# Kernel optimization log

Measured on AMD Instinct MI355X. Metric: run time of the kernel, lower is better.

The kernel has to match this reference:

```python
import jax, jax.numpy as jnp
import numpy as np

N_QUBITS = 12
DEPTH = 3


def _apply_1q(state, U, wire, n):
    # state: [B, 2^n] complex; U: [2,2] (shared) or [B,2,2] (per-sample)
    B = state.shape[0]
    a = 2 ** wire
    c = 2 ** (n - wire - 1)
    psi = state.reshape(B, a, 2, c)
    if U.ndim == 2:
        psi = jnp.einsum('ij,bajc->baic', U, psi)
    else:
        psi = jnp.einsum('bij,bajc->baic', U, psi)
    return psi.reshape(B, -1)


def _apply_cnot(state, ctrl, tgt, n):
    B = state.shape[0]
    psi = state.reshape((B,) + (2,) * n)
    psi = jnp.moveaxis(psi, (1 + ctrl, 1 + tgt), (1, 2))
    # flip target bit on the control=1 branch
    psi = jnp.concatenate([psi[:, :1], jnp.flip(psi[:, 1:], axis=2)], axis=1)
    psi = jnp.moveaxis(psi, (1, 2), (1 + ctrl, 1 + tgt))
    return psi.reshape(B, -1)


def _ry(theta):
    # theta: [B] -> [B,2,2]
    c = jnp.cos(theta / 2)
    s = jnp.sin(theta / 2)
    return jnp.stack([jnp.stack([c, -s], -1), jnp.stack([s, c], -1)], -2).astype(jnp.complex64)


def _rot(phi, theta, omega):
    # PennyLane Rot(phi, theta, omega) = RZ(omega) @ RY(theta) @ RZ(phi)
    c = jnp.cos(theta / 2).astype(jnp.complex64)
    s = jnp.sin(theta / 2).astype(jnp.complex64)
    e = lambda a: jnp.exp(1j * a.astype(jnp.complex64))
    m00 = e(-(phi + omega) / 2) * c
    m01 = -e((phi - omega) / 2) * s
    m10 = e(-(phi - omega) / 2) * s
    m11 = e((phi + omega) / 2) * c
    return jnp.stack([jnp.stack([m00, m01]), jnp.stack([m10, m11])])


def _circuit(angles, weights, n, depth):
    # angles: [B, n] real; weights: [depth, n, 3]
    B = angles.shape[0]
    state = jnp.zeros((B, 2 ** n), jnp.complex64).at[:, 0].set(1.0)
    # RY angle encoding
    for q in range(n):
        state = _apply_1q(state, _ry(angles[:, q]), q, n)
    # StronglyEntanglingLayers: Rot on each wire, then ring CNOTs with range r
    for l in range(depth):
        for q in range(n):
            U = _rot(weights[l, q, 0], weights[l, q, 1], weights[l, q, 2])
            state = _apply_1q(state, U, q, n)
        r = l % (n - 1) + 1  # PennyLane default ranges
        for q in range(n):
            state = _apply_cnot(state, q, (q + r) % n, n)
    # PauliZ expectation on each wire
    probs = state.real ** 2 + state.imag ** 2  # [B, 2^n]
    idx = jnp.arange(2 ** n)
    bits = (idx[None, :] >> (n - 1 - jnp.arange(n)[:, None])) & 1  # wire 0 = MSB
    signs = (1.0 - 2.0 * bits).astype(probs.dtype)  # [n, 2^n]
    return probs @ signs.T  # [B, n]


def setup_inputs() -> dict:
    key = jax.random.key(0)
    ks = jax.random.split(key, 5)
    B, F, n, C = 4096, 768, N_QUBITS, 10
    x = jax.random.normal(ks[0], (B, F), jnp.float32)
    Wp = jax.random.normal(ks[1], (n, F), jnp.float32) / np.sqrt(F)
    weights = 0.01 * jax.random.normal(ks[2], (DEPTH, n, 3), jnp.float32)
    Wo = jax.random.normal(ks[3], (C, n), jnp.float32) / np.sqrt(n)
    bo = jax.random.normal(ks[4], (C,), jnp.float32) * 0.01
    return {'x': x, 'Wp': Wp, 'weights': weights, 'Wo': Wo, 'bo': bo}


def reference(x, Wp, weights, Wo, bo):
    angles = jnp.tanh(x @ Wp.T) * (np.pi / 2)  # [B, n_qubits]
    z = _circuit(angles, weights, N_QUBITS, DEPTH)  # [B, n_qubits]
    return z @ Wo.T + bo  # [B, num_classes]
```

## Files before the change

### kernel.cpp

```cpp
#include <hip/hip_runtime.h>
#include <math.h>

#define NQ 12
#define DEPTH 3
#define FEAT 768
#define NCLS 10
#define NW 8
#define AMPS 8
#define PI_HALF 1.57079632679489662f

typedef float v2f __attribute__((ext_vector_type(2)));

__device__ __forceinline__ v2f pk_mul_bl(v2f A, v2f z) {
    v2f d;
    asm("v_pk_mul_f32 %0, %1, %2 op_sel:[0,0] op_sel_hi:[1,0]"
        : "=v"(d) : "v"(A), "v"(z));
    return d;
}
__device__ __forceinline__ void pk_fma_bl(v2f& d, v2f A, v2f z) {
    asm("v_pk_fma_f32 %0, %1, %2, %0 op_sel:[0,0,0] op_sel_hi:[1,0,1]"
        : "+v"(d) : "v"(A), "v"(z));
}
__device__ __forceinline__ void pk_fma_bh(v2f& d, v2f B, v2f z) {
    asm("v_pk_fma_f32 %0, %1, %2, %0 op_sel:[0,1,0] op_sel_hi:[1,1,1]"
        : "+v"(d) : "v"(B), "v"(z));
}
__device__ __forceinline__ v2f cgate(v2f As, v2f Bs, v2f Ap, v2f Bp, v2f z, v2f p) {
    v2f d = pk_mul_bl(As, z);
    pk_fma_bh(d, Bs, z);
    pk_fma_bl(d, Ap, p);
    pk_fma_bh(d, Bp, p);
    return d;
}

#define DPPF(v, ctrl) __int_as_float(__builtin_amdgcn_update_dpp(0, __float_as_int(v), (ctrl), 0xF, 0xF, true))

template<int M>
__device__ __forceinline__ float swx(float v) {
    if constexpr (M == 1) {
        return DPPF(v, 0xB1);
    } else if constexpr (M == 2) {
        return DPPF(v, 0x4E);
    } else if constexpr (M == 4) {
        float t = DPPF(v, 0x141);
        return DPPF(t, 0x1B);
    } else if constexpr (M == 8) {
        return DPPF(v, 0x128);
    } else if constexpr (M == 16) {
        return __int_as_float(__builtin_amdgcn_ds_swizzle(__float_as_int(v), 0x401F));
    } else {
        return __shfl_xor(v, 32, 64);
    }
}

template<int M>
__device__ __forceinline__ v2f swx2(v2f z) {
    v2f p;
    p.x = swx<M>(z.x);
    p.y = swx<M>(z.y);
    return p;
}

__device__ __forceinline__ float allred(float v) {
    v += swx<1>(v); v += swx<2>(v); v += swx<4>(v);
    v += swx<8>(v); v += swx<16>(v); v += swx<32>(v);
    return v;
}


template<int JM>
__device__ __forceinline__ void rot_reg(v2f (&z)[AMPS], const v2f* m) {
    const v2f A0 = m[0], B0 = m[1], P0 = m[2], Q0 = m[3];
    const v2f A1 = m[4], B1 = m[5], P1 = m[6], Q1 = m[7];
    #pragma unroll
    for (int j = 0; j < AMPS; ++j) if (!(j & JM)) {
        const int j1 = j | JM;
        v2f z0 = z[j], z1 = z[j1];
        z[j]  = cgate(A0, B0, P0, Q0, z0, z1);
        z[j1] = cgate(A1, B1, P1, Q1, z1, z0);
    }
}

template<int LM>
__device__ __forceinline__ void rot_lane(v2f (&z)[AMPS], const v2f* m, int lane) {
    const bool b = (lane & LM) != 0;
    const v2f As = b ? m[4] : m[0], Bs = b ? m[5] : m[1];
    const v2f Ap = b ? m[6] : m[2], Bp = b ? m[7] : m[3];
    #pragma unroll
    for (int j = 0; j < AMPS; ++j) {
        v2f p = swx2<LM>(z[j]);
        z[j] = cgate(As, Bs, Ap, Bp, z[j], p);
    }
}

__device__ __forceinline__ void relayout(v2f (&z)[AMPS], v2f (*ex)[AMPS][64], int lw, int lane) {
    #pragma unroll
    for (int k = 0; k < AMPS; ++k) ex[lw][k][lane] = z[k];
    __syncthreads();
    #pragma unroll
    for (int k = 0; k < AMPS; ++k) z[k] = ex[k][lw][lane];
    __syncthreads();
}

template<int JC, int JT>
__device__ __forceinline__ void cnot_rr(v2f (&z)[AMPS]) {
    #pragma unroll
    for (int j = 0; j < AMPS; ++j) if ((j & JC) && !(j & JT)) {
        const int j1 = j | JT;
        v2f t = z[j]; z[j] = z[j1]; z[j1] = t;
    }
}

__global__ __launch_bounds__(512) void qcircuit_fz(
    const float* __restrict__ x,
    const float* __restrict__ Wp,
    const float* __restrict__ w,
    const float* __restrict__ Wo,
    const float* __restrict__ bo,
    float* __restrict__ out)
{
    const int t = threadIdx.x;
    const int wave = t >> 6;
    const int lane = t & 63;
    const int b = blockIdx.x;

    __shared__ v2f mcoef[DEPTH * NQ][8];
    __shared__ v2f ex[NW][AMPS][64];
    __shared__ float red[NW][NQ];
    __shared__ float sh_dot[NQ];
    __shared__ float sh_ac[NQ], sh_as[NQ], zsh[NQ];

    if (t < DEPTH * NQ) {
        float phi = w[t * 3 + 0], th = w[t * 3 + 1], om = w[t * 3 + 2];
        float ct = cosf(0.5f * th), sn = sinf(0.5f * th);
        float a0 = -0.5f * (phi + om);
        float a1 = 0.5f * (phi - om);
        float c0 = cosf(a0), s0 = sinf(a0);
        float c1 = cosf(a1), s1 = sinf(a1);
        float m00r = c0 * ct,  m00i = s0 * ct;
        float m01r = -c1 * sn, m01i = -s1 * sn;
        float m10r = c1 * sn,  m10i = -s1 * sn;
        float m11r = c0 * ct,  m11i = -s0 * ct;
        mcoef[t][0] = v2f{m00r, m00i};  mcoef[t][1] = v2f{-m00i, m00r};
        mcoef[t][2] = v2f{m01r, m01i};  mcoef[t][3] = v2f{-m01i, m01r};
        mcoef[t][4] = v2f{m11r, m11i};  mcoef[t][5] = v2f{-m11i, m11r};
        mcoef[t][6] = v2f{m10r, m10i};  mcoef[t][7] = v2f{-m10i, m10r};
    }

    {
        const float2* x2  = reinterpret_cast<const float2*>(x + (size_t)b * FEAT);
        const float2* Wp2 = reinterpret_cast<const float2*>(Wp);
        float2 xv[6];
        #pragma unroll
        for (int c = 0; c < 6; ++c) xv[c] = x2[lane + 64 * c];
        float accA = 0.f;
        #pragma unroll
        for (int c = 0; c < 6; ++c) {
            float2 wv = Wp2[wave * 384 + lane + 64 * c];
            accA += xv[c].x * wv.x + xv[c].y * wv.y;
        }
        accA = allred(accA);
        float accB = 0.f;
        if (wave < 4) {
            #pragma unroll
            for (int c = 0; c < 6; ++c) {
                float2 wv = Wp2[(wave + 8) * 384 + lane + 64 * c];
                accB += xv[c].x * wv.x + xv[c].y * wv.y;
            }
            accB = allred(accB);
        }
        if (lane == 0) {
            sh_dot[wave] = accA;
            if (wave < 4) sh_dot[wave + 8] = accB;
        }
    }
    __syncthreads();
    if (t < NQ) {
        float h = 0.5f * (tanhf(sh_dot[t]) * PI_HALF);
        sh_ac[t] = cosf(h);
        sh_as[t] = sinf(h);
    }
    __syncthreads();

    int lw = wave;
    float pr[AMPS];
    float L0 = ((wave & 4) ? sh_as[0] : sh_ac[0]);
    L0 *= (wave & 2) ? sh_as[1] : sh_ac[1];
    L0 *= (wave & 1) ? sh_as[2] : sh_ac[2];
    L0 *= (lane & 32) ? sh_as[3] : sh_ac[3];
    L0 *= (lane & 16) ? sh_as[4] : sh_ac[4];
    L0 *= (lane &  8) ? sh_as[5] : sh_ac[5];
    L0 *= (lane &  4) ? sh_as[6] : sh_ac[6];
    L0 *= (lane &  2) ? sh_as[7] : sh_ac[7];
    L0 *= (lane &  1) ? sh_as[8] : sh_ac[8];
    pr[0] = L0;
    #pragma unroll
    for (int wbit = 0; wbit < 3; ++wbit) {
        const int bmask = 1 << wbit;
        const float cw = sh_ac[11 - wbit], sw = sh_as[11 - wbit];
        #pragma unroll
        for (int j = 0; j < AMPS; ++j) {
            if (j < bmask) {
                pr[j | bmask] = pr[j] * sw;
                pr[j] = pr[j] * cw;
            }
        }
    }
    v2f z[AMPS];
    #pragma unroll
    for (int j = 0; j < AMPS; ++j) z[j] = v2f{pr[j], 0.f};

    {
        const v2f* mb = &mcoef[0 * NQ][0];
        rot_reg < 4>(z, mb + 9 * 8);
        rot_reg < 2>(z, mb + 10 * 8);
        rot_reg < 1>(z, mb + 11 * 8);
        rot_lane<32>(z, mb + 3 * 8, lane);
        rot_lane<16>(z, mb + 4 * 8, lane);
        rot_lane< 8>(z, mb + 5 * 8, lane);
        rot_lane< 4>(z, mb + 6 * 8, lane);
        rot_lane< 2>(z, mb + 7 * 8, lane);
        rot_lane< 1>(z, mb + 8 * 8, lane);
        relayout(z, ex, lw, lane);
        rot_reg < 4>(z, mb + 0 * 8);
        rot_reg < 2>(z, mb + 1 * 8);
        rot_reg < 1>(z, mb + 2 * 8);
        cnot_rr< 4,  2>(z);
        cnot_rr< 2,  1>(z);
        {
            const int woff = (lane & 1) << 2;
            int Ls = lane;
            Ls ^= (Ls & 2) >> 1;
            Ls ^= (Ls & 4) >> 1;
            Ls ^= (Ls & 8) >> 1;
            Ls ^= (Ls & 16) >> 1;
            Ls ^= (Ls & 32) >> 1;
            int lw2 = lw ^ ((lw & 4) ? 2 : 0);
            lw2 ^= (lw2 & 2) ? 1 : 0;
            const int wlc = (lw2 & 1) << 2;
            #pragma unroll
            for (int k = 0; k < AMPS; ++k) ex[lw][k][lane] = z[k];
            __syncthreads();
            #pragma unroll
            for (int k = 0; k < AMPS; ++k)
                z[k] = ex[lw ^ woff][k ^ wlc][Ls ^ ((k & 1) << 5)];
            __syncthreads();
            lw = lw2;
        }
    }
    {
        const v2f* mb = &mcoef[1 * NQ][0];
        rot_reg < 4>(z, mb + 0 * 8);
        rot_reg < 2>(z, mb + 1 * 8);
        rot_reg < 1>(z, mb + 2 * 8);
        rot_lane<32>(z, mb + 3 * 8, lane);
        rot_lane<16>(z, mb + 4 * 8, lane);
        rot_lane< 8>(z, mb + 5 * 8, lane);
        rot_lane< 4>(z, mb + 6 * 8, lane);
        rot_lane< 2>(z, mb + 7 * 8, lane);
        rot_lane< 1>(z, mb + 8 * 8, lane);
        relayout(z, ex, lw, lane);
        rot_reg < 4>(z, mb + 9 * 8);
        rot_reg < 2>(z, mb + 10 * 8);
        rot_reg < 1>(z, mb + 11 * 8);
        {
            lw ^= (lw & 4) >> 2;
            int Ls = lane;
            Ls ^= (Ls & 4) >> 2;
            Ls ^= (Ls & 8) >> 2;
            Ls ^= (Ls & 16) >> 2;
            Ls ^= (Ls & 32) >> 2;
            const int klx = ((lane & 2) << 1) ^ ((lane & 1) << 1);
            #pragma unroll
            for (int k = 0; k < AMPS; ++k) ex[lw][k][lane] = z[k];
            __syncthreads();
            #pragma unroll
            for (int k = 0; k < AMPS; ++k) {
                const int LW = lw ^ ((k & 1) << 1) ^ ((k & 2) << 1);
                const int K  = k ^ ((k & 4) >> 2) ^ klx;
                const int Lr = Ls ^ ((LW & 1) << 4) ^ ((LW & 2) << 4);
                z[k] = ex[LW][K][Lr];
            }
            __syncthreads();
        }
    }
    {
        const v2f* mb = &mcoef[2 * NQ][0];
        rot_reg < 4>(z, mb + 9 * 8);
        rot_reg < 2>(z, mb + 10 * 8);
        rot_reg < 1>(z, mb + 11 * 8);
        rot_lane<32>(z, mb + 3 * 8, lane);
        rot_lane<16>(z, mb + 4 * 8, lane);
        rot_lane< 8>(z, mb + 5 * 8, lane);
        rot_lane< 4>(z, mb + 6 * 8, lane);
        rot_lane< 2>(z, mb + 7 * 8, lane);
        rot_lane< 1>(z, mb + 8 * 8, lane);
        relayout(z, ex, lw, lane);
        rot_reg < 4>(z, mb + 0 * 8);
        rot_reg < 2>(z, mb + 1 * 8);
        rot_reg < 1>(z, mb + 2 * 8);
    }

    float ptot = 0.f, zn4 = 0.f, zn2 = 0.f, zn1 = 0.f;
    #pragma unroll
    for (int j = 0; j < AMPS; ++j) {
        float p = z[j].x * z[j].x + z[j].y * z[j].y;
        ptot += p;
        if (j & 4) zn4 += p;
        if (j & 2) zn2 += p;
        if (j & 1) zn1 += p;
    }
    const float S4 = ptot - 2.f * zn4;
    const float S2 = ptot - 2.f * zn2;
    const float S1 = ptot - 2.f * zn1;
    const bool p36 = ((lane >> 5) ^ (lane >> 2)) & 1;
    const bool p18 = ((lane >> 4) ^ (lane >> 1)) & 1;
    const bool p9  = ((lane >> 3) ^ lane) & 1;

    const float a0 = allred(p36 ? -ptot : ptot);
    const float a1 = allred(p18 ? -ptot : ptot);
    const float a2 = allred(p9  ? -ptot : ptot);
    const float a3 = allred((lane & 32) ? -S4 : S4);
    const float a4 = allred((lane & 16) ? -S2 : S2);
    const float a5 = allred((lane &  8) ? -S1 : S1);
    const float a6 = allred(p36 ? -S4 : S4);
    const float a7 = allred(p18 ? -S2 : S2);
    const float a8 = allred(p9  ? -S1 : S1);

    const float W9  = (lw & 4) ? -1.f : 1.f;
    const float W10 = (lw & 2) ? -1.f : 1.f;
    const float W11 = (lw & 1) ? -1.f : 1.f;
    float zp[NQ];
    zp[0]  = W9 * a0;   zp[1]  = W10 * a1;  zp[2]  = W11 * a2;
    zp[3]  = a3;        zp[4]  = a4;        zp[5]  = a5;
    zp[6]  = a6;        zp[7]  = a7;        zp[8]  = a8;
    zp[9]  = W9 * a6;   zp[10] = W10 * a7;  zp[11] = W11 * a8;

    if (lane == 0) {
        #pragma unroll
        for (int q = 0; q < NQ; ++q) red[wave][q] = zp[q];
    }
    __syncthreads();
    if (t < NQ) {
        float s = 0.f;
        #pragma unroll
        for (int v = 0; v < NW; ++v) s += red[v][t];
        zsh[t] = s;
    }
    __syncthreads();

    if (t < NCLS) {
        float o = bo[t];
        #pragma unroll
        for (int q = 0; q < NQ; ++q) o = fmaf(zsh[q], Wo[t * NQ + q], o);
        out[(size_t)b * NCLS + t] = o;
    }
}

extern "C" void kernel_launch(void* const* d_in, const int* in_sizes, int n_in,
                              void* d_out, int out_size, void* d_ws, size_t ws_size,
                              hipStream_t stream) {
    const float* x  = (const float*)d_in[0];
    const float* Wp = (const float*)d_in[1];
    const float* w  = (const float*)d_in[2];
    const float* Wo = (const float*)d_in[3];
    const float* bo = (const float*)d_in[4];
    float* out = (float*)d_out;

    const int B = in_sizes[0] / FEAT;
    qcircuit_fz<<<B, 512, 0, stream>>>(x, Wp, w, Wo, bo, out);
}
```

Before: 128.9 us.

## Use ds_swizzle lane exchange, pointer-select gate coefs, and float4 projection loads

Lane-exchange butterflies in the rotation gates now use ds_swizzle (or shfl for the 32-lane stride) for every stride, replacing the DPP variants used for strides below 16. Per-lane gate coefficients are chosen by offsetting a pointer instead of selecting each value. The input projection loads x and Wp as float4 rather than float2, halving the number of load instructions. ds_swizzle goes through the LDS crossbar, so it may add latency compared with DPP, while the wider loads reduce load instruction count.

```diff
diff --git a/kernel.cpp b/kernel.cpp
--- a/kernel.cpp
+++ b/kernel.cpp
@@ -54,11 +54,19 @@
 }
 
 template<int M>
-__device__ __forceinline__ v2f swx2(v2f z) {
-    v2f p;
-    p.x = swx<M>(z.x);
-    p.y = swx<M>(z.y);
-    return p;
+__device__ __forceinline__ v2f swxd2(v2f z) {
+    if constexpr (M == 32) {
+        v2f p;
+        p.x = __shfl_xor(z.x, 32, 64);
+        p.y = __shfl_xor(z.y, 32, 64);
+        return p;
+    } else {
+        const int off = (M << 10) | 0x1F;
+        v2f p;
+        p.x = __int_as_float(__builtin_amdgcn_ds_swizzle(__float_as_int(z.x), off));
+        p.y = __int_as_float(__builtin_amdgcn_ds_swizzle(__float_as_int(z.y), off));
+        return p;
+    }
 }
 
 __device__ __forceinline__ float allred(float v) {
@@ -83,12 +91,11 @@
 
 template<int LM>
 __device__ __forceinline__ void rot_lane(v2f (&z)[AMPS], const v2f* m, int lane) {
-    const bool b = (lane & LM) != 0;
-    const v2f As = b ? m[4] : m[0], Bs = b ? m[5] : m[1];
-    const v2f Ap = b ? m[6] : m[2], Bp = b ? m[7] : m[3];
+    const v2f* mm = m + (((lane & LM) != 0) ? 4 : 0);
+    const v2f As = mm[0], Bs = mm[1], Ap = mm[2], Bp = mm[3];
     #pragma unroll
     for (int j = 0; j < AMPS; ++j) {
-        v2f p = swx2<LM>(z[j]);
+        v2f p = swxd2<LM>(z[j]);
         z[j] = cgate(As, Bs, Ap, Bp, z[j], p);
     }
 }
@@ -111,7 +118,7 @@
     }
 }
 
-__global__ __launch_bounds__(512) void qcircuit_fz(
+__global__ __launch_bounds__(512) void qcircuit_fz2(
     const float* __restrict__ x,
     const float* __restrict__ Wp,
     const float* __restrict__ w,
@@ -148,24 +155,24 @@
     }
 
     {
-        const float2* x2  = reinterpret_cast<const float2*>(x + (size_t)b * FEAT);
-        const float2* Wp2 = reinterpret_cast<const float2*>(Wp);
-        float2 xv[6];
-        #pragma unroll
-        for (int c = 0; c < 6; ++c) xv[c] = x2[lane + 64 * c];
+        const float4* x4  = reinterpret_cast<const float4*>(x + (size_t)b * FEAT);
+        const float4* Wp4 = reinterpret_cast<const float4*>(Wp);
+        float4 xv[3];
+        #pragma unroll
+        for (int c = 0; c < 3; ++c) xv[c] = x4[lane + 64 * c];
         float accA = 0.f;
         #pragma unroll
-        for (int c = 0; c < 6; ++c) {
-            float2 wv = Wp2[wave * 384 + lane + 64 * c];
-            accA += xv[c].x * wv.x + xv[c].y * wv.y;
+        for (int c = 0; c < 3; ++c) {
+            float4 wv = Wp4[wave * 192 + lane + 64 * c];
+            accA += xv[c].x * wv.x + xv[c].y * wv.y + xv[c].z * wv.z + xv[c].w * wv.w;
         }
         accA = allred(accA);
         float accB = 0.f;
         if (wave < 4) {
             #pragma unroll
-            for (int c = 0; c < 6; ++c) {
-                float2 wv = Wp2[(wave + 8) * 384 + lane + 64 * c];
-                accB += xv[c].x * wv.x + xv[c].y * wv.y;
+            for (int c = 0; c < 3; ++c) {
+                float4 wv = Wp4[(wave + 8) * 192 + lane + 64 * c];
+                accB += xv[c].x * wv.x + xv[c].y * wv.y + xv[c].z * wv.z + xv[c].w * wv.w;
             }
             accB = allred(accB);
         }
@@ -368,5 +375,5 @@
     float* out = (float*)d_out;
 
     const int B = in_sizes[0] / FEAT;
-    qcircuit_fz<<<B, 512, 0, stream>>>(x, Wp, w, Wo, bo, out);
-}
+    qcircuit_fz2<<<B, 512, 0, stream>>>(x, Wp, w, Wo, bo, out);
+}
```

Result: slower. 131.5 us (+2.0%).
